# Kernel optimization log

Hardware: AMD Instinct MI355X
Metric: run time of the kernel (lower is better)

## Reference

```python
import jax, jax.numpy as jnp
import numpy as np

B, S, D = 4, 8192, 512
H, DK = 8, 64
LOCAL_W = 256
GLOBAL_STRIDE = 64
LN_EPS = 1e-5


def setup_inputs() -> dict:
    key = jax.random.key(0)
    ks = jax.random.split(key, 9)
    scale = 1.0 / np.sqrt(D)
    def lin(k, din, dout):
        return jax.random.normal(k, (din, dout), jnp.float32) * scale
    return {
        "x": jax.random.normal(ks[0], (B, S, D), jnp.float32),
        "lq_w": lin(ks[1], D, D), "lq_b": jnp.zeros((D,), jnp.float32),
        "lk_w": lin(ks[2], D, D), "lk_b": jnp.zeros((D,), jnp.float32),
        "lv_w": lin(ks[3], D, D), "lv_b": jnp.zeros((D,), jnp.float32),
        "gq_w": lin(ks[4], D, D), "gq_b": jnp.zeros((D,), jnp.float32),
        "gk_w": lin(ks[5], D, D), "gk_b": jnp.zeros((D,), jnp.float32),
        "gv_w": lin(ks[6], D, D), "gv_b": jnp.zeros((D,), jnp.float32),
        "out_w": jax.random.normal(ks[7], (2 * D, D), jnp.float32) * (1.0 / np.sqrt(2 * D)),
        "out_b": jnp.zeros((D,), jnp.float32),
        "ln_g": jnp.ones((D,), jnp.float32),
        "ln_b": jnp.zeros((D,), jnp.float32),
    }


def _local_attention(x, qw, qb, kw, kb, vw, vb):
    # x: [B,S,D]; S divisible by LOCAL_W -> no padding path.
    nW = S // LOCAL_W
    xw = x.reshape(B, nW, LOCAL_W, D)
    def heads(w, b):
        y = jnp.einsum('bnwd,de->bnwe', xw, w) + b  # [B,nW,W,D]
        return y.reshape(B, nW, LOCAL_W, H, DK).transpose(0, 1, 3, 2, 4)  # [B,nW,H,W,dk]
    q, k, v = heads(qw, qb), heads(kw, kb), heads(vw, vb)
    scores = jnp.einsum('bnhqd,bnhkd->bnhqk', q, k) / np.sqrt(DK)
    attn = jax.nn.softmax(scores, axis=-1)
    out = jnp.einsum('bnhqk,bnhkd->bnhqd', attn, v)  # [B,nW,H,W,dk]
    return out.transpose(0, 1, 3, 2, 4).reshape(B, S, D)


def _global_attention(x, qw, qb, kw, kb, vw, vb):
    gc = x[:, ::GLOBAL_STRIDE]                       # [B,G,D]
    G = gc.shape[1]
    q = (x @ qw + qb).reshape(B, S, H, DK)           # [B,S,H,dk]
    k = (gc @ kw + kb).reshape(B, G, H, DK)
    v = (gc @ vw + vb).reshape(B, G, H, DK)
    scores = jnp.einsum('bshd,bghd->bhsg', q, k) / np.sqrt(DK)
    attn = jax.nn.softmax(scores, axis=-1)
    out = jnp.einsum('bhsg,bghd->bshd', attn, v)
    return out.reshape(B, S, D)


def reference(x, lq_w, lq_b, lk_w, lk_b, lv_w, lv_b,
              gq_w, gq_b, gk_w, gk_b, gv_w, gv_b,
              out_w, out_b, ln_g, ln_b):
    local = _local_attention(x, lq_w, lq_b, lk_w, lk_b, lv_w, lv_b)
    glob = _global_attention(x, gq_w, gq_b, gk_w, gk_b, gv_w, gv_b)
    combined = jnp.concatenate([local, glob], axis=-1) @ out_w + out_b
    h = x + combined  # dropout is identity in eval
    mu = jnp.mean(h, axis=-1, keepdims=True)
    var = jnp.var(h, axis=-1, keepdims=True)
    return (h - mu) / jnp.sqrt(var + LN_EPS) * ln_g + ln_b
```

## Files before the change

kernel.cpp:

```cpp
#include <hip/hip_runtime.h>
#include <hip/hip_bf16.h>
#include <stdint.h>

#define B_ 4
#define S_ 8192
#define D_ 512
#define H_ 8
#define DK_ 64
#define G_ 128
#define ROWS_ (B_*S_)

typedef unsigned short u16;
typedef __attribute__((ext_vector_type(8))) short short8;
typedef __attribute__((ext_vector_type(4))) short short4v;
typedef __attribute__((ext_vector_type(4))) float floatx4;

static __device__ __forceinline__ float bf2f(u16 u){
  union { uint32_t i; float f; } v; v.i = ((uint32_t)u) << 16; return v.f;
}
static __device__ __forceinline__ u16 f2bf(float f){
  union { float f; uint32_t i; } v; v.f = f;
  uint32_t u = v.i; u += 0x7fff + ((u >> 16) & 1); return (u16)(u >> 16);
}

static __device__ __forceinline__ void glds16(const u16* g, u16* l){
  __builtin_amdgcn_global_load_lds(
      (const __attribute__((address_space(1))) void*)g,
      (__attribute__((address_space(3))) void*)l, 16, 0, 0);
}

__global__ void cast_x_kernel(const float* __restrict__ x, u16* __restrict__ xb,
                              u16* __restrict__ xg, int n4){
  int i = blockIdx.x*blockDim.x + threadIdx.x;
  if (i >= n4) return;
  float4 v = ((const float4*)x)[i];
  short4v o;
  o[0] = (short)f2bf(v.x); o[1] = (short)f2bf(v.y);
  o[2] = (short)f2bf(v.z); o[3] = (short)f2bf(v.w);
  *(short4v*)(xb + (size_t)i*4) = o;
  int row = i >> 7;
  if ((row & 63) == 0){
    int b = row >> 13, g = (row & 8191) >> 6;
    *(short4v*)(xg + ((size_t)(b*G_ + g)*D_) + (i & 127)*4) = o;
  }
}

__global__ void transpose_cast_kernel(const float* __restrict__ W, u16* __restrict__ Ot, int K, int N){
  __shared__ float t[64][65];
  int n0 = blockIdx.x*64, k0 = blockIdx.y*64;
  int tx = threadIdx.x & 63, ty = threadIdx.x >> 6;
#pragma unroll
  for (int j=0;j<16;j++){ int k = ty + j*4; t[k][tx] = W[(size_t)(k0+k)*N + n0+tx]; }
  __syncthreads();
#pragma unroll
  for (int j=0;j<16;j++){ int n = ty + j*4; Ot[(size_t)(n0+n)*K + k0 + tx] = f2bf(t[tx][n]); }
}

__global__ void transpose_cast6_kernel(const float* s0, const float* s1, const float* s2,
    const float* s3, const float* s4, const float* s5,
    u16* __restrict__ WcatT, u16* __restrict__ WgT){
  __shared__ float t[64][65];
  int z = blockIdx.z;
  const float* W = (z==0)?s0:(z==1)?s1:(z==2)?s2:(z==3)?s3:(z==4)?s4:s5;
  u16* Ot = (z<4) ? (WcatT + (size_t)z*512*512) : (WgT + (size_t)(z-4)*512*512);
  int n0 = blockIdx.x*64, k0 = blockIdx.y*64;
  int tx = threadIdx.x & 63, ty = threadIdx.x >> 6;
#pragma unroll
  for (int j=0;j<16;j++){ int k = ty + j*4; t[k][tx] = W[(size_t)(k0+k)*512 + n0+tx]; }
  __syncthreads();
#pragma unroll
  for (int j=0;j<16;j++){ int n = ty + j*4; Ot[(size_t)(n0+n)*512 + k0 + tx] = f2bf(t[tx][n]); }
}

__global__ void build_bias_kernel(float* __restrict__ bcat, float* __restrict__ bg,
    const float* lq_b, const float* lk_b, const float* lv_b, const float* gq_b,
    const float* gk_b, const float* gv_b){
  int i = blockIdx.x*blockDim.x + threadIdx.x;
  if (i < 2048){
    const float* s = (i < 512) ? lq_b : (i < 1024) ? lk_b : (i < 1536) ? lv_b : gq_b;
    bcat[i] = s[i & 511];
  } else if (i < 3072){
    int j = i - 2048;
    bg[j] = (j < 512) ? gk_b[j] : gv_b[j - 512];
  }
}

template<int EPI>
__global__ __launch_bounds__(512, 1) void gemm_big(
    const u16* __restrict__ A, const u16* __restrict__ Bt,
    const float* __restrict__ bias, u16* __restrict__ C,
    const u16* __restrict__ X, int M, int N, int K)
{
  __shared__ u16 SM[4][16384];
  const int tid = threadIdx.x, lane = tid & 63, w = tid >> 6;
  const int wm = w >> 2, wn = w & 3;
  const int gx = gridDim.x;
  const int h = blockIdx.y * gx + blockIdx.x;
  const int chunk = (gx * gridDim.y) >> 3;
  const int work = (h & 7) * chunk + (h >> 3);
  const int bx = work % gx, by = work / gx;
  const int m0 = by*256, n0 = bx*256;
  const int T = K >> 5;

  const u16* gsrc[4]; int loff[4];
#pragma unroll
  for (int j = 0; j < 4; j++){
    int fb  = w*4 + j;
    int isB = fb >> 4;
    int blk = fb & 15;
    const u16* bp = isB ? Bt : A;
    int row = (isB ? n0 : m0) + blk*16 + (lane & 15);
    gsrc[j] = bp + (size_t)row * K + ((lane >> 4) * 8);
    loff[j] = fb*512;
  }

  floatx4 acc[8][4] = {};

  auto stageT = [&](int tt){
    u16* Sb_ = &SM[tt & 3][0];
#pragma unroll
    for (int j = 0; j < 4; j++) glds16(gsrc[j] + tt*32, Sb_ + loff[j]);
  };
  auto readFrags = [&](short8* Sa, short8* Sb, int slot){
    const u16* Tb = &SM[slot][0];
#pragma unroll
    for (int i=0;i<8;i++) Sa[i] = *(const short8*)(Tb + (wm*8 + i)*512 + lane*8);
#pragma unroll
    for (int j=0;j<4;j++) Sb[j] = *(const short8*)(Tb + (16 + wn*4 + j)*512 + lane*8);
  };
  auto doMfma = [&](const short8* Sa, const short8* Sb){
#pragma unroll
    for (int i=0;i<8;i++)
#pragma unroll
      for (int j=0;j<4;j++)
        acc[i][j] = __builtin_amdgcn_mfma_f32_16x16x32_bf16(Sa[i], Sb[j], acc[i][j], 0,0,0);
  };

  short8 A0[8], B0[4], A1[8], B1[4];

  stageT(0); stageT(1); stageT(2);
  asm volatile("s_waitcnt vmcnt(8)" ::: "memory");
  __builtin_amdgcn_s_barrier();
  readFrags(A0, B0, 0);

  for (int t = 0; t < T; t += 2){
    if (t + 2 < T) asm volatile("s_waitcnt vmcnt(4)" ::: "memory");
    else           asm volatile("s_waitcnt vmcnt(0)" ::: "memory");
    __builtin_amdgcn_s_barrier();
    if (t + 3 < T) stageT(t + 3);
    readFrags(A1, B1, (t + 1) & 3);
    doMfma(A0, B0);

    if (t + 3 < T) asm volatile("s_waitcnt vmcnt(4)" ::: "memory");
    else           asm volatile("s_waitcnt vmcnt(0)" ::: "memory");
    __builtin_amdgcn_s_barrier();
    if (t + 4 < T) stageT(t + 4);
    if (t + 2 < T) readFrags(A0, B0, (t + 2) & 3);
    doMfma(A1, B1);
  }

#pragma unroll
  for (int mi=0; mi<8; mi++)
#pragma unroll
    for (int nj=0; nj<4; nj++){
      int col = n0 + (wn*4 + nj)*16 + (lane & 15);
      float bv = bias[col];
#pragma unroll
      for (int ii=0; ii<4; ii++){
        size_t row = (size_t)(m0 + (wm*8 + mi)*16 + (lane>>4)*4 + ii);
        float v = acc[mi][nj][ii] + bv;
        if (EPI == 1) v += bf2f(X[row*N + col]);
        C[row*N + col] = f2bf(v);
      }
    }
}

__global__ __launch_bounds__(256) void gemm_small(
    const u16* __restrict__ A, const u16* __restrict__ Bt,
    const float* __restrict__ bias, u16* __restrict__ C,
    int M, int N, int K)
{
  __shared__ u16 As[128*32];
  __shared__ u16 Bs[128*32];
  const int tid = threadIdx.x, lane = tid & 63, w = tid >> 6;
  const int m0 = blockIdx.y*128, n0 = blockIdx.x*128;
  const int wm = (w>>1)*64, wn = (w&1)*64;
  floatx4 acc[4][4] = {};
  const int c0 = 2*w;
  const int sr = lane >> 2;
  const int sc = (lane & 3) * 8;
  const u16* ga0 = A  + (size_t)(m0 +  c0     *16 + sr)*K + sc;
  const u16* ga1 = A  + (size_t)(m0 + (c0 + 1)*16 + sr)*K + sc;
  const u16* gb0 = Bt + (size_t)(n0 +  c0     *16 + sr)*K + sc;
  const u16* gb1 = Bt + (size_t)(n0 + (c0 + 1)*16 + sr)*K + sc;
  u16* la0 = &As[ c0     *512];
  u16* la1 = &As[(c0 + 1)*512];
  u16* lb0 = &Bs[ c0     *512];
  u16* lb1 = &Bs[(c0 + 1)*512];

  for (int k0 = 0; k0 < K; k0 += 32){
    __syncthreads();
    glds16(ga0 + k0, la0);
    glds16(ga1 + k0, la1);
    glds16(gb0 + k0, lb0);
    glds16(gb1 + k0, lb1);
    __syncthreads();
    short8 af[4], bf[4];
#pragma unroll
    for (int i=0;i<4;i++) af[i] = *(const short8*)&As[(wm + i*16 + (lane&15))*32 + (lane>>4)*8];
#pragma unroll
    for (int i=0;i<4;i++) bf[i] = *(const short8*)&Bs[(wn + i*16 + (lane&15))*32 + (lane>>4)*8];
#pragma unroll
    for (int mi=0;mi<4;mi++)
#pragma unroll
      for (int ni=0;ni<4;ni++)
        acc[mi][ni] = __builtin_amdgcn_mfma_f32_16x16x32_bf16(af[mi], bf[ni], acc[mi][ni], 0,0,0);
  }

#pragma unroll
  for (int mi=0;mi<4;mi++)
#pragma unroll
    for (int ni=0;ni<4;ni++){
      int col = n0 + wn + ni*16 + (lane&15);
      float bv = bias[col];
#pragma unroll
      for (int i=0;i<4;i++){
        size_t row = (size_t)(m0 + wm + mi*16 + (lane>>4)*4 + i);
        C[row*N + col] = f2bf(acc[mi][ni][i] + bv);
      }
    }
}

template<int KVLEN, int KSTRIDE, bool GLOBAL>
__global__ __launch_bounds__(512, 4) void attn_kernel(
    const u16* __restrict__ qkv, const u16* __restrict__ kvbuf, u16* __restrict__ comb)
{
  __shared__ u16 SM[KVLEN*128 + 8192];
  u16* Kl = SM;
  u16* Vt = SM + KVLEN*64;
  u16* Pl = SM + KVLEN*128;
  const int tid = threadIdx.x, lane = tid & 63, w = tid >> 6;
  const int h = blockIdx.x, n = blockIdx.y, b = blockIdx.z;
  const size_t qrow0 = (size_t)b*S_ + (size_t)n*256;
  const int krow0 = GLOBAL ? b*G_ : (b*S_ + n*256);
  const int qc = (GLOBAL ? 1536 : 0)   + h*DK_;
  const int kc = (GLOBAL ? 0    : 512) + h*DK_;
  const int vc = (GLOBAL ? 512  : 1024)+ h*DK_;
  const int oc = (GLOBAL ? 512  : 0)   + h*DK_;
  constexpr int NC = KVLEN/64;

  {
    const int rpw = KVLEN/8;
    const int r0w = w * rpw;
    const int cg = ((lane & 7) ^ (lane >> 3)) * 8;
    const int rl = lane >> 3;
#pragma unroll
    for (int j = 0; j < rpw; j += 8){
      int row = r0w + j + rl;
      glds16(kvbuf + (size_t)(krow0 + row)*KSTRIDE + kc + cg, &Kl[(r0w + j)*64]);
    }
  }
  if (tid < (KVLEN/4)*8){
    const int rb = tid >> 3;
    const int kv0 = rb * 4;
    const int d0 = (tid & 7) * 8;
    const u16* vp = kvbuf + (size_t)(krow0 + kv0)*KSTRIDE + vc + d0;
    short8 rIn[4];
#pragma unroll
    for (int i=0;i<4;i++) rIn[i] = *(const short8*)(vp + (size_t)i*KSTRIDE);
    const int c   = rb >> 1;
    const int sub = kv0 & 7;
#pragma unroll
    for (int dd=0; dd<8; dd++){
      int d = d0 + dd;
      short4v o;
#pragma unroll
      for (int j=0;j<4;j++) o[j] = rIn[j][dd];
      *(short4v*)&Vt[d*KVLEN + ((c ^ (d&7)) << 3) + sub] = o;
    }
  }
  __syncthreads();

  const float sc2 = 0.125f * 1.44269504f;
  const int Pbase = w*16*64;

  for (int sp = 2*w; sp < 2*w + 2; sp++){
    const u16* qp = qkv + (qrow0 + sp*16 + (lane&15))*2048 + qc + ((lane>>4)*8);
    short8 qf0 = *(const short8*)qp;
    short8 qf1 = *(const short8*)(qp + 32);

    floatx4 oacc[4] = {};
    float sm[4] = {0.f,0.f,0.f,0.f};

#pragma unroll
    for (int c = 0; c < NC; c++){
      floatx4 sacc[4];
#pragma unroll
      for (int nf = 0; nf < 4; nf++){
        const u16* kb = &Kl[((c*4 + nf)*16 + (lane&15))*64];
        short8 kf0 = *(const short8*)(kb + ((( lane>>4)      ^ (lane&7)) << 3));
        short8 kf1 = *(const short8*)(kb + ((((lane>>4) + 4) ^ (lane&7)) << 3));
        floatx4 z = {0.f,0.f,0.f,0.f};
        z = __builtin_amdgcn_mfma_f32_16x16x32_bf16(qf0, kf0, z, 0,0,0);
        z = __builtin_amdgcn_mfma_f32_16x16x32_bf16(qf1, kf1, z, 0,0,0);
        sacc[nf] = z;
      }
#pragma unroll
      for (int nf=0;nf<4;nf++)
#pragma unroll
        for (int i=0;i<4;i++){
          float e = exp2f(sacc[nf][i] * sc2);
          sm[i] += e;
          int row = (lane>>4)*4 + i;
          int ch  = nf*2 + ((lane>>3)&1);
          Pl[Pbase + row*64 + ((ch ^ (row&7)) << 3) + (lane&7)] = f2bf(e);
        }
#pragma unroll
      for (int kk=0; kk<2; kk++){
        int prow = lane & 15;
        short8 pf = *(const short8*)&Pl[Pbase + prow*64 + (((kk*4 + (lane>>4)) ^ (prow&7)) << 3)];
#pragma unroll
        for (int nd=0; nd<4; nd++){
          int d = nd*16 + (lane&15);
          short8 vf = *(const short8*)&Vt[d*KVLEN + (((c*8 + kk*4 + (lane>>4)) ^ (d&7)) << 3)];
          oacc[nd] = __builtin_amdgcn_mfma_f32_16x16x32_bf16(pf, vf, oacc[nd], 0,0,0);
        }
      }
    }

#pragma unroll
    for (int i=0;i<4;i++){
#pragma unroll
      for (int msk=1; msk<16; msk<<=1) sm[i] += __shfl_xor(sm[i], msk);
      sm[i] = 1.f / sm[i];
    }
#pragma unroll
    for (int nd=0; nd<4; nd++)
#pragma unroll
      for (int i=0;i<4;i++){
        size_t row = qrow0 + sp*16 + (lane>>4)*4 + i;
        comb[row*1024 + oc + nd*16 + (lane&15)] = f2bf(oacc[nd][i] * sm[i]);
      }
  }
}

__global__ __launch_bounds__(256) void ln_kernel(const u16* __restrict__ hb,
    float* __restrict__ out, const float* __restrict__ g, const float* __restrict__ bta){
  int lane = threadIdx.x & 63, w = threadIdx.x >> 6;
  size_t row = (size_t)blockIdx.x*4 + w;
  const u16* p = hb + row*D_;
  short8 hv = *(const short8*)(p + lane*8);
  float f[8]; float s = 0.f, q = 0.f;
#pragma unroll
  for (int i=0;i<8;i++){ f[i] = bf2f((u16)hv[i]); s += f[i]; q += f[i]*f[i]; }
#pragma unroll
  for (int msk=1; msk<64; msk<<=1){ s += __shfl_xor(s, msk); q += __shfl_xor(q, msk); }
  float mean = s * (1.f/512.f);
  float var  = q * (1.f/512.f) - mean*mean;
  float inv  = rsqrtf(var + 1e-5f);
  float4 g0 = ((const float4*)g)[lane*2],   g1 = ((const float4*)g)[lane*2+1];
  float4 b0 = ((const float4*)bta)[lane*2], b1 = ((const float4*)bta)[lane*2+1];
  float4 o0, o1;
  o0.x = (f[0]-mean)*inv*g0.x + b0.x; o0.y = (f[1]-mean)*inv*g0.y + b0.y;
  o0.z = (f[2]-mean)*inv*g0.z + b0.z; o0.w = (f[3]-mean)*inv*g0.w + b0.w;
  o1.x = (f[4]-mean)*inv*g1.x + b1.x; o1.y = (f[5]-mean)*inv*g1.y + b1.y;
  o1.z = (f[6]-mean)*inv*g1.z + b1.z; o1.w = (f[7]-mean)*inv*g1.w + b1.w;
  float* op = out + row*D_;
  ((float4*)op)[lane*2]     = o0;
  ((float4*)op)[lane*2 + 1] = o1;
}

extern "C" void kernel_launch(void* const* d_in, const int* in_sizes, int n_in,
                              void* d_out, int out_size, void* d_ws, size_t ws_size,
                              hipStream_t stream)
{
  const float* x    = (const float*)d_in[0];
  const float* lq_w = (const float*)d_in[1];
  const float* lq_b = (const float*)d_in[2];
  const float* lk_w = (const float*)d_in[3];
  const float* lk_b = (const float*)d_in[4];
  const float* lv_w = (const float*)d_in[5];
  const float* lv_b = (const float*)d_in[6];
  const float* gq_w = (const float*)d_in[7];
  const float* gq_b = (const float*)d_in[8];
  const float* gk_w = (const float*)d_in[9];
  const float* gk_b = (const float*)d_in[10];
  const float* gv_w = (const float*)d_in[11];
  const float* gv_b = (const float*)d_in[12];
  const float* out_w = (const float*)d_in[13];
  const float* out_b = (const float*)d_in[14];
  const float* ln_g = (const float*)d_in[15];
  const float* ln_b = (const float*)d_in[16];

  char* ws = (char*)d_ws;
  size_t off = 0;
  auto alloc = [&](size_t bytes)->void*{ void* p = ws + off; off += (bytes + 255) & ~255ULL; return p; };
  u16*  xb    = (u16*) alloc((size_t)ROWS_*D_*2);
  u16*  xg    = (u16*) alloc((size_t)512*512*2);
  u16*  WcatT = (u16*) alloc((size_t)2048*512*2);
  u16*  WgT   = (u16*) alloc((size_t)1024*512*2);
  u16*  WoutT = (u16*) alloc((size_t)512*1024*2);
  float* bcat = (float*)alloc(2048*4);
  float* bg   = (float*)alloc(1024*4);
  u16*  qkvg  = (u16*) alloc((size_t)ROWS_*2048*2);
  u16*  gkv   = (u16*) alloc((size_t)512*1024*2);
  u16*  comb  = (u16*) alloc((size_t)ROWS_*1024*2);
  u16*  hbuf  = qkvg;

  cast_x_kernel<<<16384,256,0,stream>>>(x, xb, xg, ROWS_*D_/4);
  transpose_cast6_kernel<<<dim3(8,8,6),256,0,stream>>>(lq_w, lk_w, lv_w, gq_w, gk_w, gv_w, WcatT, WgT);
  transpose_cast_kernel<<<dim3(8,16),256,0,stream>>>(out_w, WoutT, 1024, 512);
  build_bias_kernel<<<12,256,0,stream>>>(bcat, bg, lq_b, lk_b, lv_b, gq_b, gk_b, gv_b);

  gemm_big<0><<<dim3(8,128),512,0,stream>>>(xb, WcatT, bcat, qkvg, nullptr, ROWS_, 2048, 512);
  gemm_small<<<dim3(8,4),256,0,stream>>>(xg, WgT, bg, gkv, 512, 1024, 512);

  attn_kernel<256,2048,false><<<dim3(8,32,4),512,0,stream>>>(qkvg, qkvg, comb);
  attn_kernel<128,1024,true ><<<dim3(8,32,4),512,0,stream>>>(qkvg, gkv,  comb);

  gemm_big<1><<<dim3(2,128),512,0,stream>>>(comb, WoutT, out_b, hbuf, xb,
      ROWS_, 512, 1024);
  ln_kernel<<<8192,256,0,stream>>>(hbuf, (float*)d_out, ln_g, ln_b);
}
```

Before: 263.0 us.

## Restructure GEMM main loop to stage two K-tiles per barrier

Replaces the three-deep prefetch pipeline with register double-buffered fragments by a simpler scheme. Each iteration waits for all loads, issues async loads for the next two K-tiles, then reads LDS fragments and runs the MFMAs for the current two tiles. This halves the barriers per K-step and frees the second fragment register set, which may improve occupancy or scheduling. In exchange, LDS reads no longer overlap the previous MFMA block, and the full vmcnt(0) wait gives less global-load latency hiding.

```diff
diff --git a/kernel.cpp b/kernel.cpp
--- a/kernel.cpp
+++ b/kernel.cpp
@@ -121,42 +121,40 @@
 #pragma unroll
     for (int j = 0; j < 4; j++) glds16(gsrc[j] + tt*32, Sb_ + loff[j]);
   };
-  auto readFrags = [&](short8* Sa, short8* Sb, int slot){
-    const u16* Tb = &SM[slot][0];
-#pragma unroll
-    for (int i=0;i<8;i++) Sa[i] = *(const short8*)(Tb + (wm*8 + i)*512 + lane*8);
-#pragma unroll
-    for (int j=0;j<4;j++) Sb[j] = *(const short8*)(Tb + (16 + wn*4 + j)*512 + lane*8);
-  };
-  auto doMfma = [&](const short8* Sa, const short8* Sb){
-#pragma unroll
-    for (int i=0;i<8;i++)
-#pragma unroll
-      for (int j=0;j<4;j++)
-        acc[i][j] = __builtin_amdgcn_mfma_f32_16x16x32_bf16(Sa[i], Sb[j], acc[i][j], 0,0,0);
-  };
-
-  short8 A0[8], B0[4], A1[8], B1[4];
-
-  stageT(0); stageT(1); stageT(2);
-  asm volatile("s_waitcnt vmcnt(8)" ::: "memory");
-  __builtin_amdgcn_s_barrier();
-  readFrags(A0, B0, 0);
+
+  stageT(0); stageT(1);
 
   for (int t = 0; t < T; t += 2){
-    if (t + 2 < T) asm volatile("s_waitcnt vmcnt(4)" ::: "memory");
-    else           asm volatile("s_waitcnt vmcnt(0)" ::: "memory");
+    asm volatile("s_waitcnt vmcnt(0)" ::: "memory");
     __builtin_amdgcn_s_barrier();
-    if (t + 3 < T) stageT(t + 3);
-    readFrags(A1, B1, (t + 1) & 3);
-    doMfma(A0, B0);
-
-    if (t + 3 < T) asm volatile("s_waitcnt vmcnt(4)" ::: "memory");
-    else           asm volatile("s_waitcnt vmcnt(0)" ::: "memory");
-    __builtin_amdgcn_s_barrier();
-    if (t + 4 < T) stageT(t + 4);
-    if (t + 2 < T) readFrags(A0, B0, (t + 2) & 3);
-    doMfma(A1, B1);
+    if (t + 2 < T){ stageT(t + 2); stageT(t + 3); }
+
+    {
+      const u16* Tb = &SM[t & 3][0];
+      short8 aR[8], bR[4];
+#pragma unroll
+      for (int i=0;i<8;i++) aR[i] = *(const short8*)(Tb + (wm*8 + i)*512 + lane*8);
+#pragma unroll
+      for (int j=0;j<4;j++) bR[j] = *(const short8*)(Tb + (16 + wn*4 + j)*512 + lane*8);
+#pragma unroll
+      for (int i=0;i<8;i++)
+#pragma unroll
+        for (int j=0;j<4;j++)
+          acc[i][j] = __builtin_amdgcn_mfma_f32_16x16x32_bf16(aR[i], bR[j], acc[i][j], 0,0,0);
+    }
+    {
+      const u16* Tb = &SM[(t + 1) & 3][0];
+      short8 aR[8], bR[4];
+#pragma unroll
+      for (int i=0;i<8;i++) aR[i] = *(const short8*)(Tb + (wm*8 + i)*512 + lane*8);
+#pragma unroll
+      for (int j=0;j<4;j++) bR[j] = *(const short8*)(Tb + (16 + wn*4 + j)*512 + lane*8);
+#pragma unroll
+      for (int i=0;i<8;i++)
+#pragma unroll
+        for (int j=0;j<4;j++)
+          acc[i][j] = __builtin_amdgcn_mfma_f32_16x16x32_bf16(aR[i], bR[j], acc[i][j], 0,0,0);
+    }
   }
 
 #pragma unroll
```

Result: slower. 270.9 us (+3.0%).
